# Optimization experiments

Hardware: AMD Instinct MI355X
Metric: run time of the kernel (lower is better)

## Reference

```python
import jax, jax.numpy as jnp
import numpy as np

NUM_GRAPHS = 1024
NODES = 1024          # nodes per graph (ring length)
N = NUM_GRAPHS * NODES
H = 64


def setup_inputs() -> dict:
    key = jax.random.key(0)
    ks = jax.random.split(key, 4)
    node_index = jax.random.normal(ks[0], (N, 3), dtype=jnp.float32)
    # per-graph ring edges (intended behavior of the torch code)
    i = jnp.arange(N, dtype=jnp.int64)
    g = i // NODES
    src = i
    dst = g * NODES + (i + 1) % NODES
    edge_index = jnp.stack([src, dst])  # [2, N]
    # glorot-ish weights, zero biases (PyG GCNConv default bias=True)
    W1 = jax.random.normal(ks[1], (3, H), dtype=jnp.float32) * (1.0 / np.sqrt(3.0))
    b1 = jnp.zeros((H,), dtype=jnp.float32)
    W2 = jax.random.normal(ks[2], (H, H), dtype=jnp.float32) * (1.0 / np.sqrt(H))
    b2 = jnp.zeros((H,), dtype=jnp.float32)
    Wl = jax.random.normal(ks[3], (H, 3), dtype=jnp.float32) * (1.0 / np.sqrt(H))
    bl = jnp.zeros((3,), dtype=jnp.float32)
    return {"node_index": node_index, "edge_index": edge_index,
            "W1": W1, "b1": b1, "W2": W2, "b2": b2, "Wl": Wl, "bl": bl}


def gcn_layer(x, W, b, src, dst):
    """PyG GCNConv: symmetric-normalized aggregation with self-loops.
    out[j] = sum_{i->j} (deg_i * deg_j)^-0.5 * (x_i @ W) + b
    """
    n = x.shape[0]
    h = x @ W                                   # [n, out]
    loop = jnp.arange(n, dtype=src.dtype)
    s = jnp.concatenate([src, loop])
    d = jnp.concatenate([dst, loop])
    deg = jax.ops.segment_sum(jnp.ones(d.shape[0], dtype=h.dtype), d, num_segments=n)
    dinv = jnp.where(deg > 0, jax.lax.rsqrt(jnp.maximum(deg, 1e-12)), 0.0)
    norm = dinv[s] * dinv[d]                    # [E+n]
    msg = h[s] * norm[:, None]                  # gather + scale
    out = jax.ops.segment_sum(msg, d, num_segments=n)  # scatter-add
    return out + b


def reference(node_index, edge_index, W1, b1, W2, b2, Wl, bl):
    src, dst = edge_index[0], edge_index[1]
    x = jax.nn.relu(gcn_layer(node_index, W1, b1, src, dst))
    x = jax.nn.relu(gcn_layer(x, W2, b2, src, dst))
    return x @ Wl + bl
```

## Files before the change

### kernel.cpp

```cpp
#include <hip/hip_runtime.h>

#define NPG 1024
#define NT 256

typedef short short8 __attribute__((ext_vector_type(8)));
typedef float floatx4 __attribute__((ext_vector_type(4)));
typedef unsigned int uint4v __attribute__((ext_vector_type(4)));

#define WS_W2F 0
#define WS_W1F 4096
#define WS_WLF 6144

__device__ __forceinline__ float bf2f(unsigned short u) {
    union { unsigned int i; float f; } v; v.i = ((unsigned int)u) << 16; return v.f;
}
__device__ __forceinline__ unsigned short f2bf_rne(float f) {
    union { float ff; unsigned int i; } v; v.ff = f;
    unsigned int x = v.i;
    x += 0x7fffu + ((x >> 16) & 1u);
    return (unsigned short)(x >> 16);
}
__device__ __forceinline__ unsigned int pack_bf2(float a, float b) {
    unsigned int ia = __float_as_uint(a) + 0x8000u;
    unsigned int ib = __float_as_uint(b) + 0x8000u;
    return __builtin_amdgcn_perm(ib, ia, 0x07060302u);
}
__device__ __forceinline__ int kperm(int k) {
    return ((k & 3)) | (((k >> 2) & 3) << 4) | (((k >> 4) & 3) << 2);
}

union Frag { short8 s; unsigned int u[4]; };

__global__ void gnn_prep(const float* __restrict__ W1,
                         const float* __restrict__ W2,
                         const float* __restrict__ Wl,
                         unsigned short* __restrict__ ws)
{
    int idx = blockIdx.x * NT + threadIdx.x;
    if (idx >= 7168) return;
    int l = (idx >> 3) & 63;
    int j = idx & 7;
    int c16l = l & 15, quadl = l >> 4;
    if (idx < 4096) {
        int f = idx >> 9, ct = f >> 1, kb = f & 1;
        int o  = ct * 16 + c16l;
        int k  = kperm(kb * 32 + quadl * 8 + j);
        ws[idx] = f2bf_rne(0.5f * W2[k * 64 + o]);
    } else if (idx < 6144) {
        int r = idx - 4096, ct = r >> 9;
        ws[idx] = (quadl == 0 && j < 3) ? f2bf_rne(W1[j * 64 + ct * 16 + c16l])
                                        : (unsigned short)0;
    } else {
        int r = idx - 6144, kb = r >> 9;
        int o = kb * 32 + quadl * 8 + j;
        ws[idx] = (c16l < 3) ? f2bf_rne(Wl[o * 3 + c16l]) : (unsigned short)0;
    }
}

__global__ __launch_bounds__(NT, 4)
void gnn_main(const float* __restrict__ x0,
              const float* __restrict__ b1,
              const float* __restrict__ b2,
              const float* __restrict__ bl,
              const unsigned short* __restrict__ ws,
              float* __restrict__ out)
{
    __shared__ unsigned short sX1[2][129 * 72];

    const int t    = threadIdx.x;
    const int lane = t & 63;
    const int w    = t >> 6;
    const int c16  = lane & 15;
    const int quad = lane >> 4;

    const int g     = blockIdx.x >> 2;
    const int p0A   = (blockIdx.x & 3) * 256;
    const int gbase = g * NPG;

    Frag w1f[4];
    #pragma unroll
    for (int ct = 0; ct < 4; ct++)
        w1f[ct].s = *(const short8*)(ws + WS_W1F + ct * 512 + lane * 8);
    floatx4 b1v[4];
    #pragma unroll
    for (int ct = 0; ct < 4; ct++)
        b1v[ct] = *(const floatx4*)(b1 + ct * 16 + quad * 4);

    auto layer1 = [&](int p0, unsigned short* X1) {
        #pragma unroll
        for (int s = 0; s < 2; s++) {
            const int q = 64 * s + 16 * w + c16;
            Frag bfr1;
            bfr1.u[0] = bfr1.u[1] = bfr1.u[2] = bfr1.u[3] = 0;
            if (quad == 0) {
                int n1 = (p0 - 1 + q) & (NPG - 1);
                int n0 = (n1 - 1) & (NPG - 1);
                const float* a = x0 + (gbase + n0) * 3;
                const float* b = x0 + (gbase + n1) * 3;
                bfr1.u[0] = pack_bf2(0.5f * (a[0] + b[0]), 0.5f * (a[1] + b[1]));
                bfr1.u[1] = pack_bf2(0.5f * (a[2] + b[2]), 0.0f);
            }
            floatx4 acc1[4];
            #pragma unroll
            for (int ct = 0; ct < 4; ct++) {
                acc1[ct] = b1v[ct];
                acc1[ct] = __builtin_amdgcn_mfma_f32_16x16x32_bf16(w1f[ct].s, bfr1.s, acc1[ct], 0, 0, 0);
            }
            #pragma unroll
            for (int p = 0; p < 2; p++) {
                uint4v dv;
                dv.x = pack_bf2(fmaxf(acc1[2*p  ][0], 0.0f), fmaxf(acc1[2*p  ][1], 0.0f));
                dv.y = pack_bf2(fmaxf(acc1[2*p  ][2], 0.0f), fmaxf(acc1[2*p  ][3], 0.0f));
                dv.z = pack_bf2(fmaxf(acc1[2*p+1][0], 0.0f), fmaxf(acc1[2*p+1][1], 0.0f));
                dv.w = pack_bf2(fmaxf(acc1[2*p+1][2], 0.0f), fmaxf(acc1[2*p+1][3], 0.0f));
                *(uint4v*)&X1[q * 72 + quad * 16 + p * 8] = dv;
            }
        }
        if (t < 64) {
            const float* a = x0 + (gbase + p0 + 126) * 3;
            const float* b = x0 + (gbase + p0 + 127) * 3;
            float y0c0 = 0.5f * (a[0] + b[0]);
            float y0c1 = 0.5f * (a[1] + b[1]);
            float y0c2 = 0.5f * (a[2] + b[2]);
            const unsigned short* w1r = ws + WS_W1F + (t >> 4) * 512 + (t & 15) * 8;
            float acc = b1[t];
            acc = fmaf(y0c0, bf2f(w1r[0]), acc);
            acc = fmaf(y0c1, bf2f(w1r[1]), acc);
            acc = fmaf(y0c2, bf2f(w1r[2]), acc);
            unsigned int u = __float_as_uint(fmaxf(acc, 0.0f)) + 0x8000u;
            X1[128 * 72 + kperm(t)] = (unsigned short)(u >> 16);
        }
    };

    layer1(p0A, sX1[0]);
    __syncthreads();

    short8 a2[4][2];
    #pragma unroll
    for (int ct = 0; ct < 4; ct++)
        #pragma unroll
        for (int kb = 0; kb < 2; kb++)
            a2[ct][kb] = *(const short8*)(ws + WS_W2F + (ct * 2 + kb) * 512 + lane * 8);
    Frag a3[2];
    #pragma unroll
    for (int kb = 0; kb < 2; kb++)
        a3[kb].s = *(const short8*)(ws + WS_WLF + kb * 512 + lane * 8);
    floatx4 b2v[4];
    #pragma unroll
    for (int ct = 0; ct < 4; ct++)
        b2v[ct] = *(const floatx4*)(b2 + ct * 16 + quad * 4);

    auto layer23 = [&](int p0, const unsigned short* X1) {
        #pragma unroll
        for (int s = 0; s < 2; s++) {
            const int q = 64 * s + 16 * w + c16;
            short8 brow[2][2];
            #pragma unroll
            for (int rr = 0; rr < 2; rr++)
                #pragma unroll
                for (int kb = 0; kb < 2; kb++)
                    brow[rr][kb] = *(const short8*)(&X1[(q + rr) * 72 + kb * 32 + quad * 8]);

            floatx4 acc2[4];
            #pragma unroll
            for (int ct = 0; ct < 4; ct++) {
                floatx4 z = b2v[ct];
                z = __builtin_amdgcn_mfma_f32_16x16x32_bf16(a2[ct][0], brow[0][0], z, 0, 0, 0);
                z = __builtin_amdgcn_mfma_f32_16x16x32_bf16(a2[ct][1], brow[0][1], z, 0, 0, 0);
                z = __builtin_amdgcn_mfma_f32_16x16x32_bf16(a2[ct][0], brow[1][0], z, 0, 0, 0);
                z = __builtin_amdgcn_mfma_f32_16x16x32_bf16(a2[ct][1], brow[1][1], z, 0, 0, 0);
                acc2[ct] = z;
            }

            unsigned int x2p[4][2];
            #pragma unroll
            for (int ct = 0; ct < 4; ct++) {
                x2p[ct][0] = pack_bf2(fmaxf(acc2[ct][0], 0.0f), fmaxf(acc2[ct][1], 0.0f));
                x2p[ct][1] = pack_bf2(fmaxf(acc2[ct][2], 0.0f), fmaxf(acc2[ct][3], 0.0f));
            }

            Frag b3[2];
            #pragma unroll
            for (int kb = 0; kb < 2; kb++) {
                #pragma unroll
                for (int d = 0; d < 4; d++) {
                    int src = c16 + 16 * ((2 * quad + (d >> 1)) & 3);
                    unsigned int va = (unsigned int)__shfl((int)x2p[2 * kb][d & 1], src, 64);
                    unsigned int vb = (unsigned int)__shfl((int)x2p[2 * kb + 1][d & 1], src, 64);
                    b3[kb].u[d] = (quad >> 1) ? vb : va;
                }
            }

            floatx4 acc3 = {0.0f, 0.0f, 0.0f, 0.0f};
            acc3 = __builtin_amdgcn_mfma_f32_16x16x32_bf16(a3[0].s, b3[0].s, acc3, 0, 0, 0);
            acc3 = __builtin_amdgcn_mfma_f32_16x16x32_bf16(a3[1].s, b3[1].s, acc3, 0, 0, 0);

            if (quad == 0) {
                float* po = out + (gbase + p0 + q) * 3;
                po[0] = acc3[0] + bl[0];
                po[1] = acc3[1] + bl[1];
                po[2] = acc3[2] + bl[2];
            }
        }
    };

    layer1(p0A + 128, sX1[1]);
    layer23(p0A, sX1[0]);
    __syncthreads();

    layer23(p0A + 128, sX1[1]);
}

extern "C" void kernel_launch(void* const* d_in, const int* in_sizes, int n_in,
                              void* d_out, int out_size, void* d_ws, size_t ws_size,
                              hipStream_t stream) {
    const float* x0 = (const float*)d_in[0];
    const float* W1 = (const float*)d_in[2];
    const float* b1 = (const float*)d_in[3];
    const float* W2 = (const float*)d_in[4];
    const float* b2 = (const float*)d_in[5];
    const float* Wl = (const float*)d_in[6];
    const float* bl = (const float*)d_in[7];
    unsigned short* ws = (unsigned short*)d_ws;
    float* out = (float*)d_out;

    gnn_prep<<<28, NT, 0, stream>>>(W1, W2, Wl, ws);
    gnn_main<<<4096, NT, 0, stream>>>(x0, b1, b2, bl, ws, out);
}
```

Measured before the change: 113.4 us.

## Switch to fp16 MFMA, pre-sum neighbor rows, drop shuffle transpose for final layer

Converts weights and activations from bf16 to fp16 so two neighboring X1 rows can be added with packed half arithmetic before layer 2. This halves the layer-2 MFMA count. The final projection swaps the A and B operands and reorders the Wl layout in prep, so layer-2 outputs feed the MFMA directly without the cross-lane shuffle transpose. Outputs are written from the transposed accumulator layout. fp16 has a narrower range than bf16, and summing in half precision before accumulation adds rounding error.

```diff
diff --git a/kernel.cpp b/kernel.cpp
--- a/kernel.cpp
+++ b/kernel.cpp
@@ -3,7 +3,8 @@
 #define NPG 1024
 #define NT 256
 
-typedef short short8 __attribute__((ext_vector_type(8)));
+typedef _Float16 half8 __attribute__((ext_vector_type(8)));
+typedef __fp16 fp16x2 __attribute__((ext_vector_type(2)));
 typedef float floatx4 __attribute__((ext_vector_type(4)));
 typedef unsigned int uint4v __attribute__((ext_vector_type(4)));
 
@@ -11,25 +12,22 @@
 #define WS_W1F 4096
 #define WS_WLF 6144
 
-__device__ __forceinline__ float bf2f(unsigned short u) {
-    union { unsigned int i; float f; } v; v.i = ((unsigned int)u) << 16; return v.f;
-}
-__device__ __forceinline__ unsigned short f2bf_rne(float f) {
-    union { float ff; unsigned int i; } v; v.ff = f;
-    unsigned int x = v.i;
-    x += 0x7fffu + ((x >> 16) & 1u);
-    return (unsigned short)(x >> 16);
-}
-__device__ __forceinline__ unsigned int pack_bf2(float a, float b) {
-    unsigned int ia = __float_as_uint(a) + 0x8000u;
-    unsigned int ib = __float_as_uint(b) + 0x8000u;
-    return __builtin_amdgcn_perm(ib, ia, 0x07060302u);
+__device__ __forceinline__ unsigned short f2h(float f) {
+    union { _Float16 h; unsigned short u; } v; v.h = (_Float16)f; return v.u;
+}
+__device__ __forceinline__ float h2f(unsigned short u) {
+    union { unsigned short u; _Float16 h; } v; v.u = u; return (float)v.h;
+}
+__device__ __forceinline__ unsigned int pack_h2(float a, float b) {
+    union { fp16x2 h; unsigned int u; } v;
+    v.h = __builtin_amdgcn_cvt_pkrtz(a, b);
+    return v.u;
 }
 __device__ __forceinline__ int kperm(int k) {
     return ((k & 3)) | (((k >> 2) & 3) << 4) | (((k >> 4) & 3) << 2);
 }
 
-union Frag { short8 s; unsigned int u[4]; };
+union Frag { half8 h; unsigned int u[4]; };
 
 __global__ void gnn_prep(const float* __restrict__ W1,
                          const float* __restrict__ W2,
@@ -41,20 +39,21 @@
     int l = (idx >> 3) & 63;
     int j = idx & 7;
     int c16l = l & 15, quadl = l >> 4;
+    float v;
     if (idx < 4096) {
         int f = idx >> 9, ct = f >> 1, kb = f & 1;
         int o  = ct * 16 + c16l;
         int k  = kperm(kb * 32 + quadl * 8 + j);
-        ws[idx] = f2bf_rne(0.5f * W2[k * 64 + o]);
+        v = 0.5f * W2[k * 64 + o];
     } else if (idx < 6144) {
         int r = idx - 4096, ct = r >> 9;
-        ws[idx] = (quadl == 0 && j < 3) ? f2bf_rne(W1[j * 64 + ct * 16 + c16l])
-                                        : (unsigned short)0;
+        v = (quadl == 0 && j < 3) ? W1[j * 64 + ct * 16 + c16l] : 0.0f;
     } else {
         int r = idx - 6144, kb = r >> 9;
-        int o = kb * 32 + quadl * 8 + j;
-        ws[idx] = (c16l < 3) ? f2bf_rne(Wl[o * 3 + c16l]) : (unsigned short)0;
+        int o = (2 * kb + (j >> 2)) * 16 + quadl * 4 + (j & 3);
+        v = (c16l < 3) ? Wl[o * 3 + c16l] : 0.0f;
     }
+    ws[idx] = f2h(v);
 }
 
 __global__ __launch_bounds__(NT, 4)
@@ -80,11 +79,12 @@
     Frag w1f[4];
     #pragma unroll
     for (int ct = 0; ct < 4; ct++)
-        w1f[ct].s = *(const short8*)(ws + WS_W1F + ct * 512 + lane * 8);
+        w1f[ct].h = *(const half8*)(ws + WS_W1F + ct * 512 + lane * 8);
     floatx4 b1v[4];
     #pragma unroll
     for (int ct = 0; ct < 4; ct++)
         b1v[ct] = *(const floatx4*)(b1 + ct * 16 + quad * 4);
+    const float blv = (c16 < 3) ? bl[c16] : 0.0f;
 
     auto layer1 = [&](int p0, unsigned short* X1) {
         #pragma unroll
@@ -97,22 +97,22 @@
                 int n0 = (n1 - 1) & (NPG - 1);
                 const float* a = x0 + (gbase + n0) * 3;
                 const float* b = x0 + (gbase + n1) * 3;
-                bfr1.u[0] = pack_bf2(0.5f * (a[0] + b[0]), 0.5f * (a[1] + b[1]));
-                bfr1.u[1] = pack_bf2(0.5f * (a[2] + b[2]), 0.0f);
+                bfr1.u[0] = pack_h2(0.5f * (a[0] + b[0]), 0.5f * (a[1] + b[1]));
+                bfr1.u[1] = pack_h2(0.5f * (a[2] + b[2]), 0.0f);
             }
             floatx4 acc1[4];
             #pragma unroll
             for (int ct = 0; ct < 4; ct++) {
                 acc1[ct] = b1v[ct];
-                acc1[ct] = __builtin_amdgcn_mfma_f32_16x16x32_bf16(w1f[ct].s, bfr1.s, acc1[ct], 0, 0, 0);
+                acc1[ct] = __builtin_amdgcn_mfma_f32_16x16x32_f16(w1f[ct].h, bfr1.h, acc1[ct], 0, 0, 0);
             }
             #pragma unroll
             for (int p = 0; p < 2; p++) {
                 uint4v dv;
-                dv.x = pack_bf2(fmaxf(acc1[2*p  ][0], 0.0f), fmaxf(acc1[2*p  ][1], 0.0f));
-                dv.y = pack_bf2(fmaxf(acc1[2*p  ][2], 0.0f), fmaxf(acc1[2*p  ][3], 0.0f));
-                dv.z = pack_bf2(fmaxf(acc1[2*p+1][0], 0.0f), fmaxf(acc1[2*p+1][1], 0.0f));
-                dv.w = pack_bf2(fmaxf(acc1[2*p+1][2], 0.0f), fmaxf(acc1[2*p+1][3], 0.0f));
+                dv.x = pack_h2(fmaxf(acc1[2*p  ][0], 0.0f), fmaxf(acc1[2*p  ][1], 0.0f));
+                dv.y = pack_h2(fmaxf(acc1[2*p  ][2], 0.0f), fmaxf(acc1[2*p  ][3], 0.0f));
+                dv.z = pack_h2(fmaxf(acc1[2*p+1][0], 0.0f), fmaxf(acc1[2*p+1][1], 0.0f));
+                dv.w = pack_h2(fmaxf(acc1[2*p+1][2], 0.0f), fmaxf(acc1[2*p+1][3], 0.0f));
                 *(uint4v*)&X1[q * 72 + quad * 16 + p * 8] = dv;
             }
         }
@@ -124,27 +124,26 @@
             float y0c2 = 0.5f * (a[2] + b[2]);
             const unsigned short* w1r = ws + WS_W1F + (t >> 4) * 512 + (t & 15) * 8;
             float acc = b1[t];
-            acc = fmaf(y0c0, bf2f(w1r[0]), acc);
-            acc = fmaf(y0c1, bf2f(w1r[1]), acc);
-            acc = fmaf(y0c2, bf2f(w1r[2]), acc);
-            unsigned int u = __float_as_uint(fmaxf(acc, 0.0f)) + 0x8000u;
-            X1[128 * 72 + kperm(t)] = (unsigned short)(u >> 16);
+            acc = fmaf(y0c0, h2f(w1r[0]), acc);
+            acc = fmaf(y0c1, h2f(w1r[1]), acc);
+            acc = fmaf(y0c2, h2f(w1r[2]), acc);
+            X1[128 * 72 + kperm(t)] = f2h(fmaxf(acc, 0.0f));
         }
     };
 
     layer1(p0A, sX1[0]);
     __syncthreads();
 
-    short8 a2[4][2];
+    Frag a2[4][2];
     #pragma unroll
     for (int ct = 0; ct < 4; ct++)
         #pragma unroll
         for (int kb = 0; kb < 2; kb++)
-            a2[ct][kb] = *(const short8*)(ws + WS_W2F + (ct * 2 + kb) * 512 + lane * 8);
+            a2[ct][kb].h = *(const half8*)(ws + WS_W2F + (ct * 2 + kb) * 512 + lane * 8);
     Frag a3[2];
     #pragma unroll
     for (int kb = 0; kb < 2; kb++)
-        a3[kb].s = *(const short8*)(ws + WS_WLF + kb * 512 + lane * 8);
+        a3[kb].h = *(const half8*)(ws + WS_WLF + kb * 512 + lane * 8);
     floatx4 b2v[4];
     #pragma unroll
     for (int ct = 0; ct < 4; ct++)
@@ -154,52 +153,36 @@
         #pragma unroll
         for (int s = 0; s < 2; s++) {
             const int q = 64 * s + 16 * w + c16;
-            short8 brow[2][2];
-            #pragma unroll
-            for (int rr = 0; rr < 2; rr++)
-                #pragma unroll
-                for (int kb = 0; kb < 2; kb++)
-                    brow[rr][kb] = *(const short8*)(&X1[(q + rr) * 72 + kb * 32 + quad * 8]);
-
+            half8 bsum[2];
+            #pragma unroll
+            for (int kb = 0; kb < 2; kb++) {
+                half8 r0 = *(const half8*)(&X1[(q    ) * 72 + kb * 32 + quad * 8]);
+                half8 r1 = *(const half8*)(&X1[(q + 1) * 72 + kb * 32 + quad * 8]);
+                bsum[kb] = r0 + r1;
+            }
             floatx4 acc2[4];
             #pragma unroll
             for (int ct = 0; ct < 4; ct++) {
                 floatx4 z = b2v[ct];
-                z = __builtin_amdgcn_mfma_f32_16x16x32_bf16(a2[ct][0], brow[0][0], z, 0, 0, 0);
-                z = __builtin_amdgcn_mfma_f32_16x16x32_bf16(a2[ct][1], brow[0][1], z, 0, 0, 0);
-                z = __builtin_amdgcn_mfma_f32_16x16x32_bf16(a2[ct][0], brow[1][0], z, 0, 0, 0);
-                z = __builtin_amdgcn_mfma_f32_16x16x32_bf16(a2[ct][1], brow[1][1], z, 0, 0, 0);
+                z = __builtin_amdgcn_mfma_f32_16x16x32_f16(a2[ct][0].h, bsum[0], z, 0, 0, 0);
+                z = __builtin_amdgcn_mfma_f32_16x16x32_f16(a2[ct][1].h, bsum[1], z, 0, 0, 0);
                 acc2[ct] = z;
             }
-
-            unsigned int x2p[4][2];
+            Frag pa[2];
             #pragma unroll
             for (int ct = 0; ct < 4; ct++) {
-                x2p[ct][0] = pack_bf2(fmaxf(acc2[ct][0], 0.0f), fmaxf(acc2[ct][1], 0.0f));
-                x2p[ct][1] = pack_bf2(fmaxf(acc2[ct][2], 0.0f), fmaxf(acc2[ct][3], 0.0f));
-            }
-
-            Frag b3[2];
-            #pragma unroll
-            for (int kb = 0; kb < 2; kb++) {
-                #pragma unroll
-                for (int d = 0; d < 4; d++) {
-                    int src = c16 + 16 * ((2 * quad + (d >> 1)) & 3);
-                    unsigned int va = (unsigned int)__shfl((int)x2p[2 * kb][d & 1], src, 64);
-                    unsigned int vb = (unsigned int)__shfl((int)x2p[2 * kb + 1][d & 1], src, 64);
-                    b3[kb].u[d] = (quad >> 1) ? vb : va;
-                }
-            }
-
+                pa[ct >> 1].u[(ct & 1) * 2    ] = pack_h2(fmaxf(acc2[ct][0], 0.0f), fmaxf(acc2[ct][1], 0.0f));
+                pa[ct >> 1].u[(ct & 1) * 2 + 1] = pack_h2(fmaxf(acc2[ct][2], 0.0f), fmaxf(acc2[ct][3], 0.0f));
+            }
             floatx4 acc3 = {0.0f, 0.0f, 0.0f, 0.0f};
-            acc3 = __builtin_amdgcn_mfma_f32_16x16x32_bf16(a3[0].s, b3[0].s, acc3, 0, 0, 0);
-            acc3 = __builtin_amdgcn_mfma_f32_16x16x32_bf16(a3[1].s, b3[1].s, acc3, 0, 0, 0);
-
-            if (quad == 0) {
-                float* po = out + (gbase + p0 + q) * 3;
-                po[0] = acc3[0] + bl[0];
-                po[1] = acc3[1] + bl[1];
-                po[2] = acc3[2] + bl[2];
+            acc3 = __builtin_amdgcn_mfma_f32_16x16x32_f16(pa[0].h, a3[0].h, acc3, 0, 0, 0);
+            acc3 = __builtin_amdgcn_mfma_f32_16x16x32_f16(pa[1].h, a3[1].h, acc3, 0, 0, 0);
+            if (c16 < 3) {
+                float* po = out + (gbase + p0 + 64 * s + 16 * w + quad * 4) * 3 + c16;
+                po[0] = acc3[0] + blv;
+                po[3] = acc3[1] + blv;
+                po[6] = acc3[2] + blv;
+                po[9] = acc3[3] + blv;
             }
         }
     };
```

Result: faster. 107.5 us (-5.2%).
